# Kernel tuning notes

Measured on AMD Instinct MI355X. Metric: run time of the kernel, lower is better.

The kernel has to match this reference:

```python
import jax, jax.numpy as jnp
import numpy as np

N = 100000
E = 1600000
IN_C, HID_C, OUT_C = 128, 64, 64


def setup_inputs() -> dict:
    key = jax.random.key(0)
    k1, k2, k3, k4, k5 = jax.random.split(key, 5)
    x = jax.random.normal(k1, (N, IN_C), dtype=jnp.float32)
    edge_index = jax.random.randint(k2, (2, E), 0, N, dtype=jnp.int64)
    # Glorot-style params per GCNConv (weight [in,out], bias [out])
    W1 = jax.random.normal(k3, (IN_C, HID_C), dtype=jnp.float32) / np.sqrt(IN_C)
    b1 = jnp.zeros((HID_C,), dtype=jnp.float32)
    W2 = jax.random.normal(k4, (HID_C, OUT_C), dtype=jnp.float32) / np.sqrt(HID_C)
    b2 = jnp.zeros((OUT_C,), dtype=jnp.float32)
    return {"x": x, "edge_index": edge_index, "W1": W1, "b1": b1, "W2": W2, "b2": b2}


def _gcn_norm(edge_index, n):
    # add self-loops, then symmetric normalization deg^{-1/2} A deg^{-1/2}
    loop = jnp.arange(n, dtype=edge_index.dtype)
    src = jnp.concatenate([edge_index[0], loop])
    dst = jnp.concatenate([edge_index[1], loop])
    deg = jax.ops.segment_sum(jnp.ones_like(dst, dtype=jnp.float32), dst, num_segments=n)
    dinv = jnp.where(deg > 0, jax.lax.rsqrt(deg), 0.0)
    norm = dinv[src] * dinv[dst]  # [E+N]
    return src, dst, norm


def _gcn_conv(x, W, b, src, dst, norm, n):
    h = x @ W                                   # [N, out]
    m = h[src] * norm[:, None]                  # gather + scale  [E+N, out]
    out = jax.ops.segment_sum(m, dst, num_segments=n)  # scatter-add at dst
    return out + b


def reference(x, edge_index, W1, b1, W2, b2):
    n = x.shape[0]
    src, dst, norm = _gcn_norm(edge_index, n)
    h = jax.nn.relu(_gcn_conv(x, W1, b1, src, dst, norm, n))
    out = _gcn_conv(h, W2, b2, src, dst, norm, n)
    return out
```

## Files before the change

kernel.cpp:

```cpp
#include <hip/hip_runtime.h>
#include <hip/hip_fp16.h>


#define CAP   64
#define CAPB  3072
#define BKMAX 1024

typedef _Float16 f16x8 __attribute__((ext_vector_type(8)));
typedef float f32x4 __attribute__((ext_vector_type(4)));

struct alignas(8) H4 { __half2 a, b; };
struct alignas(16) H8 { __half2 a, b, c, d; };
__device__ inline H4 pack4(float x, float y, float z, float w) {
  H4 r; r.a = __floats2half2_rn(x, y); r.b = __floats2half2_rn(z, w); return r;
}

__global__ void detect_i64_kernel(const unsigned int* __restrict__ w, int ncheck,
                                  int* __restrict__ flag) {
  __shared__ int nz;
  if (threadIdx.x == 0) nz = 0;
  __syncthreads();
  for (int i = threadIdx.x; i < ncheck; i += blockDim.x) {
    if (w[2 * i + 1] != 0u) nz = 1;
  }
  __syncthreads();
  if (threadIdx.x == 0) flag[0] = (nz == 0) ? 1 : 0;
}

__global__ __launch_bounds__(256) void hist_gemm_kernel(
    const int* __restrict__ edges, int E, const int* __restrict__ flag,
    int* __restrict__ Hh, int SB, int nbk,
    int* __restrict__ tmp_pk, int* __restrict__ tmp_mt,
    const float* __restrict__ A, const float* __restrict__ W,
    __half* __restrict__ g, int n) {
  __shared__ __align__(16) char smem[34816];
  const int t = threadIdx.x;
  const int bid = (int)blockIdx.x;

  if (bid < SB) {
    int* hist = (int*)smem;
    const int f = flag[0];
    const int blk0 = bid * 2048;

    for (int i = t; i < nbk; i += 256) hist[i] = 0;
    __syncthreads();

    if (blk0 + 2048 <= E) {
      int sv[8], dv[8];
      if (f) {
#pragma unroll
        for (int u = 0; u < 4; ++u) {
          const int eg = blk0 + (u * 256 + t) * 2;
          const int4 a = *(const int4*)&edges[2 * (size_t)eg];
          const int4 b = *(const int4*)&edges[2 * ((size_t)E + eg)];
          sv[u * 2] = a.x; sv[u * 2 + 1] = a.z;
          dv[u * 2] = b.x; dv[u * 2 + 1] = b.z;
        }
      } else {
#pragma unroll
        for (int u = 0; u < 2; ++u) {
          const int eg = blk0 + (u * 256 + t) * 4;
          const int4 a = *(const int4*)&edges[eg];
          const int4 b = *(const int4*)&edges[(size_t)E + eg];
          sv[u * 4] = a.x; sv[u * 4 + 1] = a.y; sv[u * 4 + 2] = a.z; sv[u * 4 + 3] = a.w;
          dv[u * 4] = b.x; dv[u * 4 + 1] = b.y; dv[u * 4 + 2] = b.z; dv[u * 4 + 3] = b.w;
        }
      }
      int pk[8], mt[8];
#pragma unroll
      for (int i = 0; i < 8; ++i) {
        const int bk = dv[i] >> 7;
        const int rk = atomicAdd(&hist[bk], 1);
        pk[i] = ((dv[i] & 127) << 17) | sv[i];
        mt[i] = bk | (rk << 10);
      }
      if (f) {
#pragma unroll
        for (int u = 0; u < 4; ++u) {
          const int eg = blk0 + (u * 256 + t) * 2;
          *(int2*)&tmp_pk[eg] = make_int2(pk[u * 2], pk[u * 2 + 1]);
          *(int2*)&tmp_mt[eg] = make_int2(mt[u * 2], mt[u * 2 + 1]);
        }
      } else {
        *(int4*)&tmp_pk[blk0 + t * 4]        = make_int4(pk[0], pk[1], pk[2], pk[3]);
        *(int4*)&tmp_pk[blk0 + 1024 + t * 4] = make_int4(pk[4], pk[5], pk[6], pk[7]);
        *(int4*)&tmp_mt[blk0 + t * 4]        = make_int4(mt[0], mt[1], mt[2], mt[3]);
        *(int4*)&tmp_mt[blk0 + 1024 + t * 4] = make_int4(mt[4], mt[5], mt[6], mt[7]);
      }
    } else {
      for (int e = blk0 + t; e < E; e += 256) {
        const int s = f ? edges[2 * (size_t)e] : edges[e];
        const int d = f ? edges[2 * ((size_t)E + e)] : edges[(size_t)E + e];
        const int bk = d >> 7;
        const int rk = atomicAdd(&hist[bk], 1);
        tmp_pk[e] = ((d & 127) << 17) | s;
        tmp_mt[e] = bk | (rk << 10);
      }
    }
    __syncthreads();
    for (int i = t; i < nbk; i += 256) Hh[(size_t)i * SB + bid] = hist[i];
    return;
  }

  _Float16 (*Af)[136] = (_Float16(*)[136])smem;
  _Float16 (*Wf)[136] = (_Float16(*)[136])(smem + 17408);
  const int row0 = (bid - SB) * 64;

  {
    const int r = t >> 2, k0 = (t & 3) << 5;
    const int gr = row0 + r;
    if (gr < n) {
#pragma unroll
      for (int q = 0; q < 4; ++q) {
        float4 a = *(const float4*)&A[(size_t)gr * 128 + k0 + q * 8];
        float4 b = *(const float4*)&A[(size_t)gr * 128 + k0 + q * 8 + 4];
        f16x8 v;
        v[0] = (_Float16)a.x; v[1] = (_Float16)a.y; v[2] = (_Float16)a.z; v[3] = (_Float16)a.w;
        v[4] = (_Float16)b.x; v[5] = (_Float16)b.y; v[6] = (_Float16)b.z; v[7] = (_Float16)b.w;
        *(f16x8*)&Af[r][k0 + q * 8] = v;
      }
    } else {
      f16x8 z = {0, 0, 0, 0, 0, 0, 0, 0};
#pragma unroll
      for (int q = 0; q < 4; ++q) *(f16x8*)&Af[r][k0 + q * 8] = z;
    }
  }
  {
    const int c = t & 63, kq = t >> 6;
#pragma unroll
    for (int i = 0; i < 32; ++i)
      Wf[c][kq * 32 + i] = (_Float16)W[(size_t)(kq * 32 + i) * 64 + c];
  }
  __syncthreads();

  const int wid = t >> 6, lane = t & 63;
  const int lr = lane & 15, kg = lane >> 4;
  f32x4 acc[4] = {{0, 0, 0, 0}, {0, 0, 0, 0}, {0, 0, 0, 0}, {0, 0, 0, 0}};
#pragma unroll
  for (int kc = 0; kc < 4; ++kc) {
    f16x8 av = *(const f16x8*)&Af[wid * 16 + lr][kc * 32 + kg * 8];
#pragma unroll
    for (int ct = 0; ct < 4; ++ct) {
      f16x8 bv = *(const f16x8*)&Wf[ct * 16 + lr][kc * 32 + kg * 8];
      acc[ct] = __builtin_amdgcn_mfma_f32_16x16x32_f16(av, bv, acc[ct], 0, 0, 0);
    }
  }
#pragma unroll
  for (int ct = 0; ct < 4; ++ct) {
#pragma unroll
    for (int rg = 0; rg < 4; ++rg) {
      const int r = row0 + wid * 16 + kg * 4 + rg;
      if (r < n) g[(size_t)r * 64 + ct * 16 + lr] = (__half)(float)acc[ct][rg];
    }
  }
}

__global__ __launch_bounds__(256) void scan_hist_kernel(
    int* __restrict__ Hh, int SB, int* __restrict__ T) {
  __shared__ int sm[256];
  __shared__ int carry;
  const int b = blockIdx.x;
  const int t = threadIdx.x;
  if (t == 0) carry = 0;
  __syncthreads();
  int* __restrict__ row = Hh + (size_t)b * SB;
  for (int base = 0; base < SB; base += 256) {
    const int i = base + t;
    const int v = (i < SB) ? row[i] : 0;
    sm[t] = v;
    __syncthreads();
    for (int off = 1; off < 256; off <<= 1) {
      int u = (t >= off) ? sm[t - off] : 0;
      __syncthreads();
      sm[t] += u;
      __syncthreads();
    }
    const int excl = sm[t] - v + carry;
    if (i < SB) row[i] = excl;
    __syncthreads();
    if (t == 0) carry += sm[255];
    __syncthreads();
  }
  if (t == 0) T[b] = carry;
}

__global__ __launch_bounds__(256) void place_kernel(
    const int* __restrict__ tmp_pk, const int* __restrict__ tmp_mt,
    const int* __restrict__ Hh, int SB, int E, int* __restrict__ arena) {
  const int e0 = ((int)blockIdx.x * 256 + (int)threadIdx.x) * 4;
  if (e0 >= E) return;
  const int blk = e0 >> 11;
  if (e0 + 4 <= E) {
    const int4 pk = *(const int4*)&tmp_pk[e0];
    const int4 mt = *(const int4*)&tmp_mt[e0];
    const int b0 = mt.x & 1023, b1 = mt.y & 1023, b2 = mt.z & 1023, b3 = mt.w & 1023;
    const int p0 = Hh[(size_t)b0 * SB + blk] + (mt.x >> 10);
    const int p1 = Hh[(size_t)b1 * SB + blk] + (mt.y >> 10);
    const int p2 = Hh[(size_t)b2 * SB + blk] + (mt.z >> 10);
    const int p3 = Hh[(size_t)b3 * SB + blk] + (mt.w >> 10);
    if (p0 < CAPB) arena[(size_t)b0 * CAPB + p0] = pk.x;
    if (p1 < CAPB) arena[(size_t)b1 * CAPB + p1] = pk.y;
    if (p2 < CAPB) arena[(size_t)b2 * CAPB + p2] = pk.z;
    if (p3 < CAPB) arena[(size_t)b3 * CAPB + p3] = pk.w;
  } else {
    for (int e = e0; e < E; ++e) {
      const int mt = tmp_mt[e];
      const int bk = mt & 1023;
      const int p = Hh[(size_t)bk * SB + blk] + (mt >> 10);
      if (p < CAPB) arena[(size_t)bk * CAPB + p] = tmp_pk[e];
    }
  }
}

__global__ __launch_bounds__(512) void cluster_csr_kernel(
    const int* __restrict__ T, const int* __restrict__ arena,
    int n, int* __restrict__ counts, float* __restrict__ dinv,
    int* __restrict__ csrp) {
  __shared__ int lc[128];
  const int b = blockIdx.x;
  const int t = threadIdx.x;
  if (t < 128) lc[t] = 0;
  __syncthreads();
  int cnt = T[b];
  if (cnt > CAPB) cnt = CAPB;
  const int* __restrict__ seg = &arena[(size_t)b * CAPB];
  for (int j = t; j < cnt; j += 512) {
    const int p = seg[j];
    const int dl = p >> 17;
    const int s = p & 131071;
    const int r = atomicAdd(&lc[dl], 1);
    if (r < CAP) csrp[((size_t)(b << 7) + dl) * CAP + r] = s;
  }
  __syncthreads();
  const int d = (b << 7) + t;
  if (t < 128 && d < n) {
    counts[d] = lc[t];
    dinv[d] = rsqrtf((float)(lc[t] + 1));
  }
}

__global__ __launch_bounds__(256) void gemm2_kernel(
    const _Float16* __restrict__ h, const float* __restrict__ W,
    const float* __restrict__ dinv, __half* __restrict__ out, int n) {
  __shared__ __align__(16) _Float16 Af[64][72];
  __shared__ __align__(16) _Float16 Wf[64][72];
  const int t = threadIdx.x;
  const int row0 = blockIdx.x * 64;

  {
    const int r = t >> 2, k0 = (t & 3) << 4;
    const int gr = row0 + r;
    if (gr < n) {
      *(f16x8*)&Af[r][k0] = *(const f16x8*)&h[(size_t)gr * 64 + k0];
      *(f16x8*)&Af[r][k0 + 8] = *(const f16x8*)&h[(size_t)gr * 64 + k0 + 8];
    } else {
      f16x8 z = {0, 0, 0, 0, 0, 0, 0, 0};
      *(f16x8*)&Af[r][k0] = z;
      *(f16x8*)&Af[r][k0 + 8] = z;
    }
  }
  {
    const int c = t & 63, kq = t >> 6;
#pragma unroll
    for (int i = 0; i < 16; ++i)
      Wf[c][kq * 16 + i] = (_Float16)W[(size_t)(kq * 16 + i) * 64 + c];
  }
  __syncthreads();

  const int wid = t >> 6, lane = t & 63;
  const int lr = lane & 15, kg = lane >> 4;
  f32x4 acc[4] = {{0, 0, 0, 0}, {0, 0, 0, 0}, {0, 0, 0, 0}, {0, 0, 0, 0}};
#pragma unroll
  for (int kc = 0; kc < 2; ++kc) {
    f16x8 av = *(const f16x8*)&Af[wid * 16 + lr][kc * 32 + kg * 8];
#pragma unroll
    for (int ct = 0; ct < 4; ++ct) {
      f16x8 bv = *(const f16x8*)&Wf[ct * 16 + lr][kc * 32 + kg * 8];
      acc[ct] = __builtin_amdgcn_mfma_f32_16x16x32_f16(av, bv, acc[ct], 0, 0, 0);
    }
  }
  float sc[4];
#pragma unroll
  for (int rg = 0; rg < 4; ++rg) {
    const int r = row0 + wid * 16 + kg * 4 + rg;
    sc[rg] = (r < n) ? dinv[r] : 0.f;
  }
#pragma unroll
  for (int ct = 0; ct < 4; ++ct) {
#pragma unroll
    for (int rg = 0; rg < 4; ++rg) {
      const int r = row0 + wid * 16 + kg * 4 + rg;
      if (r < n) out[(size_t)r * 64 + ct * 16 + lr] = (__half)((float)acc[ct][rg] * sc[rg]);
    }
  }
}

template <bool EDGE_SCALE, bool RELU, typename OUT>
__global__ __launch_bounds__(256) void agg_kernel(
    const __half* __restrict__ hs, const int* __restrict__ counts,
    const int* __restrict__ csrp, const float* __restrict__ dinv,
    const float* __restrict__ bias, OUT* __restrict__ out, int n) {
  const int wid = blockIdx.x * 4 + ((int)threadIdx.x >> 6);
  if (wid * 8 >= n) return;
  const int lane = (int)threadIdx.x & 63;
  const int og = lane >> 3;
  const int gl = lane & 7;
  const int d = wid * 8 + og;
  const bool active = d < n;
  const int dc = active ? d : n - 1;

  int len = counts[dc];
  if (len > CAP) len = CAP;
  if (!active) len = 0;
  const int* __restrict__ row = &csrp[(size_t)dc * CAP];
  const float dd = dinv[dc];

  H8 sv = *(const H8*)&hs[(size_t)dc * 64 + (gl << 3)];
  const float ws = EDGE_SCALE ? dd : 1.f;
  float acc[8];
  {
    float2 f0 = __half22float2(sv.a), f1 = __half22float2(sv.b);
    float2 f2 = __half22float2(sv.c), f3 = __half22float2(sv.d);
    acc[0] = ws * f0.x; acc[1] = ws * f0.y; acc[2] = ws * f1.x; acc[3] = ws * f1.y;
    acc[4] = ws * f2.x; acc[5] = ws * f2.y; acc[6] = ws * f3.x; acc[7] = ws * f3.y;
  }

  for (int j = 0; __any(j < len); j += 8) {
    int sidx[8];
    bool pr[8];
#pragma unroll
    for (int u = 0; u < 8; ++u) {
      pr[u] = (j + u) < len;
      sidx[u] = pr[u] ? row[j + u] : dc;
    }
    H8 v[8];
#pragma unroll
    for (int u = 0; u < 8; ++u) v[u] = *(const H8*)&hs[(size_t)sidx[u] * 64 + (gl << 3)];
#pragma unroll
    for (int u = 0; u < 8; ++u) {
      const float w = pr[u] ? (EDGE_SCALE ? dinv[sidx[u]] : 1.f) : 0.f;
      float2 g0 = __half22float2(v[u].a), g1 = __half22float2(v[u].b);
      float2 g2 = __half22float2(v[u].c), g3 = __half22float2(v[u].d);
      acc[0] = fmaf(w, g0.x, acc[0]); acc[1] = fmaf(w, g0.y, acc[1]);
      acc[2] = fmaf(w, g1.x, acc[2]); acc[3] = fmaf(w, g1.y, acc[3]);
      acc[4] = fmaf(w, g2.x, acc[4]); acc[5] = fmaf(w, g2.y, acc[5]);
      acc[6] = fmaf(w, g3.x, acc[6]); acc[7] = fmaf(w, g3.y, acc[7]);
    }
  }

  if (active) {
    const float4 b0 = *(const float4*)&bias[gl << 3];
    const float4 b1 = *(const float4*)&bias[(gl << 3) + 4];
    float o[8];
    o[0] = fmaf(acc[0], dd, b0.x); o[1] = fmaf(acc[1], dd, b0.y);
    o[2] = fmaf(acc[2], dd, b0.z); o[3] = fmaf(acc[3], dd, b0.w);
    o[4] = fmaf(acc[4], dd, b1.x); o[5] = fmaf(acc[5], dd, b1.y);
    o[6] = fmaf(acc[6], dd, b1.z); o[7] = fmaf(acc[7], dd, b1.w);
    if (RELU) {
#pragma unroll
      for (int c = 0; c < 8; ++c) o[c] = fmaxf(o[c], 0.f);
    }
    if constexpr (sizeof(OUT) == 2) {
      H8 hv;
      hv.a = __floats2half2_rn(o[0], o[1]); hv.b = __floats2half2_rn(o[2], o[3]);
      hv.c = __floats2half2_rn(o[4], o[5]); hv.d = __floats2half2_rn(o[6], o[7]);
      *(H8*)&out[(size_t)d * 64 + (gl << 3)] = hv;
    } else {
      *(float4*)&out[(size_t)d * 64 + (gl << 3)] = make_float4(o[0], o[1], o[2], o[3]);
      *(float4*)&out[(size_t)d * 64 + (gl << 3) + 4] = make_float4(o[4], o[5], o[6], o[7]);
    }
  }
}

extern "C" void kernel_launch(void* const* d_in, const int* in_sizes, int n_in,
                              void* d_out, int out_size, void* d_ws, size_t ws_size,
                              hipStream_t stream) {
  const float* x  = (const float*)d_in[0];
  const int*   ei = (const int*)d_in[1];
  const float* W1 = (const float*)d_in[2];
  const float* b1 = (const float*)d_in[3];
  const float* W2 = (const float*)d_in[4];
  const float* b2 = (const float*)d_in[5];
  float* out = (float*)d_out;

  const int N = in_sizes[0] / 128;
  const int E = in_sizes[1] / 2;
  const int NBK = (N + 127) >> 7;
  const int SB = (E + 2047) / 2048;
  const int G1 = (N + 63) / 64;

  char* ws = (char*)d_ws;
  size_t off = 0;
  auto take = [&](size_t bytes) -> void* {
    void* p = ws + off;
    off += (bytes + 255) & ~(size_t)255;
    return p;
  };
  int*    flag   = (int*)take(sizeof(int));
  int*    Hh     = (int*)take((size_t)NBK * SB * 4);
  int*    T      = (int*)take((size_t)NBK * 4);
  int*    counts = (int*)take((size_t)N * 4);
  float*  dinv   = (float*)take((size_t)N * 4);
  int*    tmp_pk = (int*)take((size_t)E * 4);
  int*    tmp_mt = (int*)take((size_t)E * 4);
  int*    arena  = (int*)take((size_t)NBK * CAPB * 4);
  int*    csrp   = (int*)take((size_t)N * CAP * 4);
  __half* hsf    = (__half*)take((size_t)N * 64 * 2);
  __half* hh     = (__half*)take((size_t)N * 64 * 2);
  (void)ws_size; (void)n_in; (void)out_size;

  detect_i64_kernel<<<1, 256, 0, stream>>>((const unsigned int*)ei, 4096, flag);

  hist_gemm_kernel<<<SB + G1, 256, 0, stream>>>(
      ei, E, flag, Hh, SB, NBK, tmp_pk, tmp_mt, x, W1, hsf, N);

  scan_hist_kernel<<<NBK, 256, 0, stream>>>(Hh, SB, T);

  place_kernel<<<((E + 3) / 4 + 255) / 256, 256, 0, stream>>>(
      tmp_pk, tmp_mt, Hh, SB, E, arena);

  cluster_csr_kernel<<<NBK, 512, 0, stream>>>(T, arena, N, counts, dinv, csrp);

  agg_kernel<true, true, __half><<<(N + 31) / 32, 256, 0, stream>>>(
      hsf, counts, csrp, dinv, b1, hh, N);

  gemm2_kernel<<<G1, 256, 0, stream>>>((const _Float16*)hh, W2, dinv, hsf, N);

  agg_kernel<false, false, float><<<(N + 31) / 32, 256, 0, stream>>>(
      hsf, counts, csrp, dinv, b2, out, N);
}
```

Before: 154.5 us.

## Fuse second GEMM into second aggregation by aggregating before multiplying

Layer two is reordered to aggregate first and multiply afterwards, using linearity (A·(hW) = (A·h)W). The separate gemm2 kernel and its fp16 intermediate write and read are removed. Each block now aggregates 32 rows of hh into shared memory and applies W2 with MFMA before writing the fp32 output plus bias. The cost is that every block reloads and converts W2 into shared memory and adds a barrier, and rounding to fp16 now happens at a different point.

```diff
diff --git a/kernel.cpp b/kernel.cpp
--- a/kernel.cpp
+++ b/kernel.cpp
@@ -9,11 +9,7 @@
 typedef _Float16 f16x8 __attribute__((ext_vector_type(8)));
 typedef float f32x4 __attribute__((ext_vector_type(4)));
 
-struct alignas(8) H4 { __half2 a, b; };
 struct alignas(16) H8 { __half2 a, b, c, d; };
-__device__ inline H4 pack4(float x, float y, float z, float w) {
-  H4 r; r.a = __floats2half2_rn(x, y); r.b = __floats2half2_rn(z, w); return r;
-}
 
 __global__ void detect_i64_kernel(const unsigned int* __restrict__ w, int ncheck,
                                   int* __restrict__ flag) {
@@ -239,67 +235,10 @@
   }
 }
 
-__global__ __launch_bounds__(256) void gemm2_kernel(
-    const _Float16* __restrict__ h, const float* __restrict__ W,
-    const float* __restrict__ dinv, __half* __restrict__ out, int n) {
-  __shared__ __align__(16) _Float16 Af[64][72];
-  __shared__ __align__(16) _Float16 Wf[64][72];
-  const int t = threadIdx.x;
-  const int row0 = blockIdx.x * 64;
-
-  {
-    const int r = t >> 2, k0 = (t & 3) << 4;
-    const int gr = row0 + r;
-    if (gr < n) {
-      *(f16x8*)&Af[r][k0] = *(const f16x8*)&h[(size_t)gr * 64 + k0];
-      *(f16x8*)&Af[r][k0 + 8] = *(const f16x8*)&h[(size_t)gr * 64 + k0 + 8];
-    } else {
-      f16x8 z = {0, 0, 0, 0, 0, 0, 0, 0};
-      *(f16x8*)&Af[r][k0] = z;
-      *(f16x8*)&Af[r][k0 + 8] = z;
-    }
-  }
-  {
-    const int c = t & 63, kq = t >> 6;
-#pragma unroll
-    for (int i = 0; i < 16; ++i)
-      Wf[c][kq * 16 + i] = (_Float16)W[(size_t)(kq * 16 + i) * 64 + c];
-  }
-  __syncthreads();
-
-  const int wid = t >> 6, lane = t & 63;
-  const int lr = lane & 15, kg = lane >> 4;
-  f32x4 acc[4] = {{0, 0, 0, 0}, {0, 0, 0, 0}, {0, 0, 0, 0}, {0, 0, 0, 0}};
-#pragma unroll
-  for (int kc = 0; kc < 2; ++kc) {
-    f16x8 av = *(const f16x8*)&Af[wid * 16 + lr][kc * 32 + kg * 8];
-#pragma unroll
-    for (int ct = 0; ct < 4; ++ct) {
-      f16x8 bv = *(const f16x8*)&Wf[ct * 16 + lr][kc * 32 + kg * 8];
-      acc[ct] = __builtin_amdgcn_mfma_f32_16x16x32_f16(av, bv, acc[ct], 0, 0, 0);
-    }
-  }
-  float sc[4];
-#pragma unroll
-  for (int rg = 0; rg < 4; ++rg) {
-    const int r = row0 + wid * 16 + kg * 4 + rg;
-    sc[rg] = (r < n) ? dinv[r] : 0.f;
-  }
-#pragma unroll
-  for (int ct = 0; ct < 4; ++ct) {
-#pragma unroll
-    for (int rg = 0; rg < 4; ++rg) {
-      const int r = row0 + wid * 16 + kg * 4 + rg;
-      if (r < n) out[(size_t)r * 64 + ct * 16 + lr] = (__half)((float)acc[ct][rg] * sc[rg]);
-    }
-  }
-}
-
-template <bool EDGE_SCALE, bool RELU, typename OUT>
-__global__ __launch_bounds__(256) void agg_kernel(
+__global__ __launch_bounds__(256) void agg1_kernel(
     const __half* __restrict__ hs, const int* __restrict__ counts,
     const int* __restrict__ csrp, const float* __restrict__ dinv,
-    const float* __restrict__ bias, OUT* __restrict__ out, int n) {
+    const float* __restrict__ bias, __half* __restrict__ out, int n) {
   const int wid = blockIdx.x * 4 + ((int)threadIdx.x >> 6);
   if (wid * 8 >= n) return;
   const int lane = (int)threadIdx.x & 63;
@@ -316,13 +255,12 @@
   const float dd = dinv[dc];
 
   H8 sv = *(const H8*)&hs[(size_t)dc * 64 + (gl << 3)];
-  const float ws = EDGE_SCALE ? dd : 1.f;
   float acc[8];
   {
     float2 f0 = __half22float2(sv.a), f1 = __half22float2(sv.b);
     float2 f2 = __half22float2(sv.c), f3 = __half22float2(sv.d);
-    acc[0] = ws * f0.x; acc[1] = ws * f0.y; acc[2] = ws * f1.x; acc[3] = ws * f1.y;
-    acc[4] = ws * f2.x; acc[5] = ws * f2.y; acc[6] = ws * f3.x; acc[7] = ws * f3.y;
+    acc[0] = dd * f0.x; acc[1] = dd * f0.y; acc[2] = dd * f1.x; acc[3] = dd * f1.y;
+    acc[4] = dd * f2.x; acc[5] = dd * f2.y; acc[6] = dd * f3.x; acc[7] = dd * f3.y;
   }
 
   for (int j = 0; __any(j < len); j += 8) {
@@ -338,7 +276,7 @@
     for (int u = 0; u < 8; ++u) v[u] = *(const H8*)&hs[(size_t)sidx[u] * 64 + (gl << 3)];
 #pragma unroll
     for (int u = 0; u < 8; ++u) {
-      const float w = pr[u] ? (EDGE_SCALE ? dinv[sidx[u]] : 1.f) : 0.f;
+      const float w = pr[u] ? dinv[sidx[u]] : 0.f;
       float2 g0 = __half22float2(v[u].a), g1 = __half22float2(v[u].b);
       float2 g2 = __half22float2(v[u].c), g3 = __half22float2(v[u].d);
       acc[0] = fmaf(w, g0.x, acc[0]); acc[1] = fmaf(w, g0.y, acc[1]);
@@ -356,18 +294,104 @@
     o[2] = fmaf(acc[2], dd, b0.z); o[3] = fmaf(acc[3], dd, b0.w);
     o[4] = fmaf(acc[4], dd, b1.x); o[5] = fmaf(acc[5], dd, b1.y);
     o[6] = fmaf(acc[6], dd, b1.z); o[7] = fmaf(acc[7], dd, b1.w);
-    if (RELU) {
-#pragma unroll
-      for (int c = 0; c < 8; ++c) o[c] = fmaxf(o[c], 0.f);
-    }
-    if constexpr (sizeof(OUT) == 2) {
-      H8 hv;
-      hv.a = __floats2half2_rn(o[0], o[1]); hv.b = __floats2half2_rn(o[2], o[3]);
-      hv.c = __floats2half2_rn(o[4], o[5]); hv.d = __floats2half2_rn(o[6], o[7]);
-      *(H8*)&out[(size_t)d * 64 + (gl << 3)] = hv;
-    } else {
-      *(float4*)&out[(size_t)d * 64 + (gl << 3)] = make_float4(o[0], o[1], o[2], o[3]);
-      *(float4*)&out[(size_t)d * 64 + (gl << 3) + 4] = make_float4(o[4], o[5], o[6], o[7]);
+#pragma unroll
+    for (int c = 0; c < 8; ++c) o[c] = fmaxf(o[c], 0.f);
+    H8 hv;
+    hv.a = __floats2half2_rn(o[0], o[1]); hv.b = __floats2half2_rn(o[2], o[3]);
+    hv.c = __floats2half2_rn(o[4], o[5]); hv.d = __floats2half2_rn(o[6], o[7]);
+    *(H8*)&out[(size_t)d * 64 + (gl << 3)] = hv;
+  }
+}
+
+__global__ __launch_bounds__(256) void agg2_gemm_kernel(
+    const __half* __restrict__ hh, const int* __restrict__ counts,
+    const int* __restrict__ csrp, const float* __restrict__ dinv,
+    const float* __restrict__ W2, const float* __restrict__ b2,
+    float* __restrict__ out, int n) {
+  __shared__ __align__(16) _Float16 Wf[64][88];
+  __shared__ __align__(16) _Float16 Ac[32][88];
+  const int t = threadIdx.x;
+
+  {
+    const int c = t & 63, kq = t >> 6;
+#pragma unroll
+    for (int i = 0; i < 16; ++i)
+      Wf[c][kq * 16 + i] = (_Float16)W2[(size_t)(kq * 16 + i) * 64 + c];
+  }
+
+  const int wid = t >> 6;
+  const int lane = t & 63;
+  const int og = lane >> 3, gl = lane & 7;
+  const int node0 = (int)blockIdx.x * 32;
+  const int d = node0 + wid * 8 + og;
+  const bool active = d < n;
+  const int dc = active ? d : n - 1;
+
+  int len = counts[dc];
+  if (len > CAP) len = CAP;
+  if (!active) len = 0;
+  const int* __restrict__ row = &csrp[(size_t)dc * CAP];
+  const float dd = dinv[dc];
+
+  H8 sv = *(const H8*)&hh[(size_t)dc * 64 + (gl << 3)];
+  float acc[8];
+  {
+    float2 f0 = __half22float2(sv.a), f1 = __half22float2(sv.b);
+    float2 f2 = __half22float2(sv.c), f3 = __half22float2(sv.d);
+    acc[0] = dd * f0.x; acc[1] = dd * f0.y; acc[2] = dd * f1.x; acc[3] = dd * f1.y;
+    acc[4] = dd * f2.x; acc[5] = dd * f2.y; acc[6] = dd * f3.x; acc[7] = dd * f3.y;
+  }
+
+  for (int j = 0; __any(j < len); j += 8) {
+    int sidx[8];
+    bool pr[8];
+#pragma unroll
+    for (int u = 0; u < 8; ++u) {
+      pr[u] = (j + u) < len;
+      sidx[u] = pr[u] ? row[j + u] : dc;
+    }
+    H8 v[8];
+#pragma unroll
+    for (int u = 0; u < 8; ++u) v[u] = *(const H8*)&hh[(size_t)sidx[u] * 64 + (gl << 3)];
+#pragma unroll
+    for (int u = 0; u < 8; ++u) {
+      const float w = pr[u] ? dinv[sidx[u]] : 0.f;
+      float2 g0 = __half22float2(v[u].a), g1 = __half22float2(v[u].b);
+      float2 g2 = __half22float2(v[u].c), g3 = __half22float2(v[u].d);
+      acc[0] = fmaf(w, g0.x, acc[0]); acc[1] = fmaf(w, g0.y, acc[1]);
+      acc[2] = fmaf(w, g1.x, acc[2]); acc[3] = fmaf(w, g1.y, acc[3]);
+      acc[4] = fmaf(w, g2.x, acc[4]); acc[5] = fmaf(w, g2.y, acc[5]);
+      acc[6] = fmaf(w, g3.x, acc[6]); acc[7] = fmaf(w, g3.y, acc[7]);
+    }
+  }
+
+  {
+    const int lrow = wid * 8 + og;
+    f16x8 av;
+#pragma unroll
+    for (int c = 0; c < 8; ++c) av[c] = (_Float16)(acc[c] * dd);
+    *(f16x8*)&Ac[lrow][gl << 3] = av;
+  }
+  __syncthreads();
+
+  const int lr = lane & 15, kg = lane >> 4;
+  const int rt = wid >> 1;
+  const int ct0 = (wid & 1) * 2;
+#pragma unroll
+  for (int cti = 0; cti < 2; ++cti) {
+    const int ct = ct0 + cti;
+    f32x4 c4 = {0, 0, 0, 0};
+#pragma unroll
+    for (int kc = 0; kc < 2; ++kc) {
+      f16x8 a = *(const f16x8*)&Ac[rt * 16 + lr][kc * 32 + kg * 8];
+      f16x8 b = *(const f16x8*)&Wf[ct * 16 + lr][kc * 32 + kg * 8];
+      c4 = __builtin_amdgcn_mfma_f32_16x16x32_f16(a, b, c4, 0, 0, 0);
+    }
+    const float bb = b2[ct * 16 + lr];
+#pragma unroll
+    for (int rg = 0; rg < 4; ++rg) {
+      const int r = node0 + rt * 16 + kg * 4 + rg;
+      if (r < n) out[(size_t)r * 64 + ct * 16 + lr] = (float)c4[rg] + bb;
     }
   }
 }
@@ -421,11 +445,9 @@
 
   cluster_csr_kernel<<<NBK, 512, 0, stream>>>(T, arena, N, counts, dinv, csrp);
 
-  agg_kernel<true, true, __half><<<(N + 31) / 32, 256, 0, stream>>>(
+  agg1_kernel<<<(N + 31) / 32, 256, 0, stream>>>(
       hsf, counts, csrp, dinv, b1, hh, N);
 
-  gemm2_kernel<<<G1, 256, 0, stream>>>((const _Float16*)hh, W2, dinv, hsf, N);
-
-  agg_kernel<false, false, float><<<(N + 31) / 32, 256, 0, stream>>>(
-      hsf, counts, csrp, dinv, b2, out, N);
-}
+  agg2_gemm_kernel<<<(N + 31) / 32, 256, 0, stream>>>(
+      hh, counts, csrp, dinv, W2, b2, out, N);
+}
```

New measurement: 147.6 us (median of 2 runs). -4.5%, faster.
